# Kernel tuning notes

Measured on AMD Instinct MI355X. Metric: run time of the kernel, lower is better.

## Reference

```python
import jax, jax.numpy as jnp
import numpy as np
import math

B, L, IN_K, IN_V = 4, 2048, 256, 256
HID, HEADS, OUT = 1024, 8, 256
D = HID // HEADS  # head_dim = 128


def setup_inputs() -> dict:
    key = jax.random.key(0)
    ks = jax.random.split(key, 9)
    s = 0.02
    return {
        "KEY": jax.random.normal(ks[0], (B, L, IN_K), jnp.float32),
        "VALUE": jax.random.normal(ks[1], (B, L, IN_V), jnp.float32),
        "QUERY": jax.random.normal(ks[2], (B, L, IN_K), jnp.float32),
        "W_w": jax.random.normal(ks[3], (HID, IN_K), jnp.float32) * s,
        "W_b": jax.random.normal(ks[4], (HID,), jnp.float32) * s,
        "Wv_w": jax.random.normal(ks[5], (HID, IN_V), jnp.float32) * s,
        "Wv_b": jax.random.normal(ks[6], (HID,), jnp.float32) * s,
        "Wo_w": jax.random.normal(ks[7], (OUT, HID), jnp.float32) * s,
        "Wo_b": jax.random.normal(ks[8], (OUT,), jnp.float32) * s,
    }


def _split_heads(x, b, l):
    # reshape hidden -> (head_dim, num_heads) [head LAST, as in source], then
    # permute(0,3,1,2) -> [B, heads, L, head_dim]
    return x.reshape(b, l, D, HEADS).transpose(0, 3, 1, 2)


def reference(KEY, VALUE, QUERY, W_w, W_b, Wv_w, Wv_b, Wo_w, Wo_b):
    b, lk, _ = KEY.shape
    lq = QUERY.shape[1]
    # shared projection W for KEY and QUERY
    Wk = _split_heads(KEY @ W_w.T + W_b, b, lk)      # [B,h,Lk,d]
    Wq = _split_heads(QUERY @ W_w.T + W_b, b, lq)    # [B,h,Lq,d]
    Wv = _split_heads(VALUE @ Wv_w.T + Wv_b, b, lk)  # [B,h,Lk,d]
    # score[b,h,i,k] = sum_j Wk[b,h,i,j] * Wq[b,h,k,j]
    score = jnp.einsum('bhij,bhkj->bhik', Wk, Wq) / math.sqrt(D)
    # NON-STANDARD: softmax over the HEAD dimension (dim=1)
    attn = jax.nn.softmax(score, axis=1)             # [B,h,Lk,Lq]
    out = jnp.einsum('bhik,bhij->bhjk', attn, Wv)    # [B,h,d,Lq]
    out = out.transpose(0, 2, 1, 3)                  # [B,d,h,Lq]
    out = out.reshape(b, D * HEADS, lq)              # [B,hidden,Lq]
    out = jnp.swapaxes(out, 2, 1)                    # [B,Lq,hidden]
    # dropout is identity in eval mode
    return out @ Wo_w.T + Wo_b                       # [B,Lq,output_size]
```

## Files before the change

kernel.cpp:

```cpp
#include <hip/hip_runtime.h>
#include <hip/hip_bf16.h>
#include <stdint.h>

#define B_    4
#define L_    2048
#define INK   256
#define HID   1024
#define NH    8
#define DH    128
#define OUTF  256

typedef __bf16 v8bf __attribute__((ext_vector_type(8)));
typedef float  v4f  __attribute__((ext_vector_type(4)));

#define MFMA(a,b,c) __builtin_amdgcn_mfma_f32_16x16x32_bf16((a),(b),(c),0,0,0)

__device__ __forceinline__ void gl_lds16(const void* gsrc, void* ldsbase) {
  __builtin_amdgcn_global_load_lds(
      (const __attribute__((address_space(1))) unsigned int*)(uintptr_t)gsrc,
      (__attribute__((address_space(3))) unsigned int*)(uint32_t)(uintptr_t)ldsbase,
      16, 0, 0);
}
__device__ __forceinline__ void wait_vm0()  { asm volatile("s_waitcnt vmcnt(0)" ::: "memory"); }
__device__ __forceinline__ void wait_vm8()  { asm volatile("s_waitcnt vmcnt(8)" ::: "memory"); }
__device__ __forceinline__ void wait_lgkm0(){ asm volatile("s_waitcnt lgkmcnt(0)" ::: "memory"); }
__device__ __forceinline__ void barrier_lgkm() {
  asm volatile("s_waitcnt lgkmcnt(0)\n\ts_barrier" ::: "memory");
}

__device__ __forceinline__ unsigned short bfbits(float f) {
  __bf16 h = (__bf16)f;
  return __builtin_bit_cast(unsigned short, h);
}
__device__ __forceinline__ unsigned pack2(float a, float b) {
  return (unsigned)bfbits(a) | ((unsigned)bfbits(b) << 16);
}

struct ConvArgs {
  const float* src[5];
  __bf16* dst[5];
  int n[5];
};
__global__ __launch_bounds__(256)
void convert_kernel(ConvArgs a) {
  const int r = blockIdx.y;
  const int i = (blockIdx.x * 256 + threadIdx.x) * 4;
  if (i >= a.n[r]) return;
  const float4 v = *(const float4*)(a.src[r] + i);
  uint2 w;
  w.x = pack2(v.x, v.y);
  w.y = pack2(v.z, v.w);
  *reinterpret_cast<uint2*>(a.dst[r] + i) = w;
}

__global__ __launch_bounds__(256)
void wo_perm_kernel(const float* __restrict__ Wo, __bf16* __restrict__ Wop) {
  const int o = blockIdx.x;
  const int hidp = threadIdx.x * 4;
  const int h = hidp >> 7, dd = hidp & 127;
  const float* src = Wo + (size_t)o * HID;
  const float v0 = src[(dd + 0) * 8 + h];
  const float v1 = src[(dd + 1) * 8 + h];
  const float v2 = src[(dd + 2) * 8 + h];
  const float v3 = src[(dd + 3) * 8 + h];
  uint2 w;
  w.x = pack2(v0, v1);
  w.y = pack2(v2, v3);
  *reinterpret_cast<uint2*>(Wop + (size_t)o * HID + hidp) = w;
}

template<int MODE>
__global__ __launch_bounds__(256, 2)
void proj_kernel(const __bf16* __restrict__ X, const __bf16* __restrict__ W,
                 const float* __restrict__ bias, __bf16* __restrict__ out)
{
  __shared__ __bf16 sA[2][128 * 64];
  __shared__ __bf16 sB[2][128 * 64];
  const int tid  = threadIdx.x;
  const int lane = tid & 63;
  const int wid  = tid >> 6;
  const int l15  = lane & 15;
  const int q    = lane >> 4;
  const int mblk = blockIdx.x * 128;
  const int nblk = blockIdx.y * 128;

  v4f acc[4][4];
  const v4f vz = {0.f, 0.f, 0.f, 0.f};
#pragma unroll
  for (int i = 0; i < 4; i++)
#pragma unroll
    for (int j = 0; j < 4; j++) acc[i][j] = vz;

  const char* Ab = (const char*)X + (size_t)mblk * 512;
  const char* Bb = (const char*)W + (size_t)nblk * 512;

  auto stage = [&](int p, int c) {
    const int koff = c * 128;
#pragma unroll
    for (int j = 0; j < 4; j++) {
      const int slot = j * 256 + tid;
      const int row = slot >> 3, g = slot & 7;
      gl_lds16(Ab + (size_t)row * 512 + koff + ((g ^ (row & 7)) << 4),
               &sA[p][(j * 256 + wid * 64) * 8]);
    }
#pragma unroll
    for (int j = 0; j < 4; j++) {
      const int slot = j * 256 + tid;
      const int row = slot >> 3, g = slot & 7;
      gl_lds16(Bb + (size_t)row * 512 + koff + ((g ^ (row & 7)) << 4),
               &sB[p][(j * 256 + wid * 64) * 8]);
    }
  };

  stage(0, 0);
  __syncthreads();
#pragma unroll
  for (int c = 0; c < 4; c++) {
    const int p = c & 1;
    if (c + 1 < 4) stage(1 - p, c + 1);
#pragma unroll
    for (int s = 0; s < 2; s++) {
      v8bf a[4], b[4];
#pragma unroll
      for (int t = 0; t < 4; t++) {
        const int row = (wid & 1) * 64 + t * 16 + l15;
        a[t] = *(const v8bf*)&sA[p][(row << 6) + (((s * 4 + q) ^ (row & 7)) << 3)];
      }
#pragma unroll
      for (int t = 0; t < 4; t++) {
        const int row = (wid >> 1) * 64 + t * 16 + l15;
        b[t] = *(const v8bf*)&sB[p][(row << 6) + (((s * 4 + q) ^ (row & 7)) << 3)];
      }
#pragma unroll
      for (int tm = 0; tm < 4; tm++)
#pragma unroll
        for (int tn = 0; tn < 4; tn++)
          acc[tm][tn] = MFMA(a[tm], b[tn], acc[tm][tn]);
    }
    __syncthreads();
  }

#pragma unroll
  for (int tn = 0; tn < 4; tn++) {
    const int n = nblk + (wid >> 1) * 64 + tn * 16 + l15;
    const float bv = bias[n];
    const int h = n & 7;
    const int dd = n >> 3;
#pragma unroll
    for (int tm = 0; tm < 4; tm++)
#pragma unroll
      for (int r = 0; r < 4; r++) {
        const int m = mblk + (wid & 1) * 64 + tm * 16 + q * 4 + r;
        const int b = m >> 11;
        const int i = m & (L_ - 1);
        const float v = acc[tm][tn][r] + bv;
        size_t idx;
        if (MODE == 0) idx = ((size_t)(b * NH + h) * L_ + i) * DH + dd;
        else           idx = ((size_t)(b * NH + h) * DH + dd) * L_ + i;
        out[idx] = (__bf16)v;
      }
  }
}

__global__ __launch_bounds__(512, 2)
void fused_attn_kernel(const __bf16* __restrict__ Kp,
                       const __bf16* __restrict__ Qp,
                       const __bf16* __restrict__ Vpt,
                       __bf16* __restrict__ Hd)
{
  extern __shared__ char smem[];
  char* sK = smem;
  char* sV = smem + 65536;
  char* sP = smem + 131072;

  const int tid  = threadIdx.x;
  const int lane = tid & 63;
  const int h    = tid >> 6;
  const int l15  = lane & 15;
  const int q    = lane >> 4;
  const int k0   = blockIdx.x * 32;
  const int b    = blockIdx.y;

  const char* KpH = (const char*)Kp  + (size_t)(b * NH + h) * L_ * DH * 2;
  const char* QpH = (const char*)Qp  + (size_t)(b * NH + h) * L_ * DH * 2;
  const char* VpH = (const char*)Vpt + (size_t)(b * NH + h) * DH * L_ * 2;
  char* sKh = sK + h * 8192;
  char* sVh = sV + h * 8192;
  char* sPh = sP + h * 2048;

  auto stage_K = [&](int i0) {
#pragma unroll
    for (int j = 0; j < 8; j++) {
      const int slot = j * 64 + lane;
      const int row = slot >> 4, g = slot & 15;
      gl_lds16(KpH + (size_t)(i0 + row) * 256 + ((g ^ (row & 15)) << 4),
               sKh + j * 1024);
    }
  };
  auto stage_V = [&](int i0) {
#pragma unroll
    for (int j = 0; j < 8; j++) {
      const int slot = j * 64 + lane;
      const int row = slot >> 2, g = slot & 3;
      gl_lds16(VpH + (size_t)row * 4096 + (size_t)i0 * 2 + ((g ^ (row & 3)) << 4),
               sVh + j * 1024);
    }
  };

  stage_K(0);
  stage_V(0);

  v8bf qf[2][4];
#pragma unroll
  for (int n = 0; n < 2; n++)
#pragma unroll
    for (int c = 0; c < 4; c++)
      qf[n][c] = *(const v8bf*)(QpH + (size_t)(k0 + n * 16 + l15) * 256 + c * 64 + q * 16);

  v4f cacc[8][2];
  const v4f vz = {0.f, 0.f, 0.f, 0.f};
#pragma unroll
  for (int t = 0; t < 8; t++)
#pragma unroll
    for (int n = 0; n < 2; n++) cacc[t][n] = vz;

  const float c2 = 0.12751744f;
  const int ip = tid & 15;
  const int kk = tid >> 4;

  for (int it = 0; it < 64; ++it) {
    const int i0 = it * 32;
    wait_vm8();

    v8bf ka[2][4];
#pragma unroll
    for (int si = 0; si < 2; si++)
#pragma unroll
      for (int c = 0; c < 4; c++) {
        const int row = si * 16 + l15;
        ka[si][c] = *(const v8bf*)(sKh + row * 256 + (((c * 4 + q) ^ l15) << 4));
      }
    wait_lgkm0();
    if (it + 1 < 64) stage_K(i0 + 32);

    v4f s[2][2];
#pragma unroll
    for (int si = 0; si < 2; si++)
#pragma unroll
      for (int n = 0; n < 2; n++) s[si][n] = vz;
#pragma unroll
    for (int c = 0; c < 4; c++)
#pragma unroll
      for (int si = 0; si < 2; si++)
#pragma unroll
        for (int n = 0; n < 2; n++)
          s[si][n] = MFMA(ka[si][c], qf[n][c], s[si][n]);

#pragma unroll
    for (int si = 0; si < 2; si++)
#pragma unroll
      for (int n = 0; n < 2; n++) {
        const float p0 = exp2f(s[si][n][0] * c2);
        const float p1 = exp2f(s[si][n][1] * c2);
        const float p2 = exp2f(s[si][n][2] * c2);
        const float p3 = exp2f(s[si][n][3] * c2);
        uint2 w;
        w.x = pack2(p0, p1);
        w.y = pack2(p2, p3);
        *(uint2*)(sPh + (n * 16 + l15) * 64 + (si * 16 + q * 4) * 2) = w;
      }
    barrier_lgkm();

    {
      unsigned u[8];
      float lo[8], hi[8], s0 = 0.f, s1 = 0.f;
#pragma unroll
      for (int hh = 0; hh < 8; hh++)
        u[hh] = *(const unsigned*)(sP + hh * 2048 + kk * 64 + ip * 4);
#pragma unroll
      for (int hh = 0; hh < 8; hh++) {
        lo[hh] = __builtin_bit_cast(float, u[hh] << 16);
        hi[hh] = __builtin_bit_cast(float, u[hh] & 0xFFFF0000u);
        s0 += lo[hh];
        s1 += hi[hh];
      }
      const float r0 = __builtin_amdgcn_rcpf(s0);
      const float r1 = __builtin_amdgcn_rcpf(s1);
#pragma unroll
      for (int hh = 0; hh < 8; hh++)
        *(unsigned*)(sP + hh * 2048 + kk * 64 + ip * 4) = pack2(lo[hh] * r0, hi[hh] * r1);
    }
    barrier_lgkm();

    v8bf va[8], pb[2];
#pragma unroll
    for (int t = 0; t < 8; t++) {
      const int row = t * 16 + l15;
      va[t] = *(const v8bf*)(sVh + row * 64 + ((q ^ (row & 3)) << 4));
    }
#pragma unroll
    for (int n = 0; n < 2; n++)
      pb[n] = *(const v8bf*)(sPh + (n * 16 + l15) * 64 + q * 16);
    wait_lgkm0();
    if (it + 1 < 64) stage_V(i0 + 32);
    else wait_vm0();
#pragma unroll
    for (int t = 0; t < 8; t++)
#pragma unroll
      for (int n = 0; n < 2; n++)
        cacc[t][n] = MFMA(va[t], pb[n], cacc[t][n]);
  }

#pragma unroll
  for (int t = 0; t < 8; t++)
#pragma unroll
    for (int n = 0; n < 2; n++) {
      uint2 w;
      w.x = pack2(cacc[t][n][0], cacc[t][n][1]);
      w.y = pack2(cacc[t][n][2], cacc[t][n][3]);
      char* dst = (char*)Hd +
          (((size_t)(b * L_ + k0 + n * 16 + l15)) * HID + h * DH + t * 16 + q * 4) * 2;
      *(uint2*)dst = w;
    }
}

__global__ __launch_bounds__(256, 2)
void outproj_kernel(const __bf16* __restrict__ Hd, const __bf16* __restrict__ Wop,
                    const float* __restrict__ bo, float* __restrict__ out)
{
  __shared__ __bf16 sA[2][64 * 64];
  __shared__ __bf16 sB[2][64 * 64];
  const int tid  = threadIdx.x;
  const int lane = tid & 63;
  const int wid  = tid >> 6;
  const int l15  = lane & 15;
  const int q    = lane >> 4;
  const int mblk = blockIdx.x * 64;
  const int nblk = blockIdx.y * 64;

  const char* Ab = (const char*)Hd  + (size_t)mblk * 2048;
  const char* Bb = (const char*)Wop + (size_t)nblk * 2048;

  auto stage = [&](int p, int c) {
#pragma unroll
    for (int j = 0; j < 2; j++) {
      const int slot = j * 256 + tid;
      const int row = slot >> 3, g = slot & 7;
      gl_lds16(Ab + (size_t)row * 2048 + c * 128 + ((g ^ (row & 7)) << 4),
               &sA[p][(j * 256 + wid * 64) * 8]);
    }
#pragma unroll
    for (int j = 0; j < 2; j++) {
      const int slot = j * 256 + tid;
      const int row = slot >> 3, g = slot & 7;
      gl_lds16(Bb + (size_t)row * 2048 + c * 128 + ((g ^ (row & 7)) << 4),
               &sB[p][(j * 256 + wid * 64) * 8]);
    }
  };

  v4f acc[2][2];
  const v4f vz = {0.f, 0.f, 0.f, 0.f};
#pragma unroll
  for (int i = 0; i < 2; i++)
#pragma unroll
    for (int j = 0; j < 2; j++) acc[i][j] = vz;

  stage(0, 0);
  __syncthreads();
#pragma unroll 1
  for (int c = 0; c < 16; c++) {
    const int p = c & 1;
    if (c + 1 < 16) stage(1 - p, c + 1);
#pragma unroll
    for (int s = 0; s < 2; s++) {
      v8bf a[2], bb[2];
#pragma unroll
      for (int t = 0; t < 2; t++) {
        const int row = (wid & 1) * 32 + t * 16 + l15;
        a[t] = *(const v8bf*)&sA[p][(row << 6) + (((s * 4 + q) ^ (row & 7)) << 3)];
      }
#pragma unroll
      for (int t = 0; t < 2; t++) {
        const int row = (wid >> 1) * 32 + t * 16 + l15;
        bb[t] = *(const v8bf*)&sB[p][(row << 6) + (((s * 4 + q) ^ (row & 7)) << 3)];
      }
#pragma unroll
      for (int tm = 0; tm < 2; tm++)
#pragma unroll
        for (int tn = 0; tn < 2; tn++)
          acc[tm][tn] = MFMA(a[tm], bb[tn], acc[tm][tn]);
    }
    __syncthreads();
  }

#pragma unroll
  for (int tn = 0; tn < 2; tn++) {
    const int n = nblk + (wid >> 1) * 32 + tn * 16 + l15;
    const float bv = bo[n];
#pragma unroll
    for (int tm = 0; tm < 2; tm++)
#pragma unroll
      for (int r = 0; r < 4; r++) {
        const int m = mblk + (wid & 1) * 32 + tm * 16 + q * 4 + r;
        out[(size_t)m * OUTF + n] = acc[tm][tn][r] + bv;
      }
  }
}

extern "C" void kernel_launch(void* const* d_in, const int* in_sizes, int n_in,
                              void* d_out, int out_size, void* d_ws, size_t ws_size,
                              hipStream_t stream) {
  const float* KEY   = (const float*)d_in[0];
  const float* VALUE = (const float*)d_in[1];
  const float* QUERY = (const float*)d_in[2];
  const float* W_w   = (const float*)d_in[3];
  const float* W_b   = (const float*)d_in[4];
  const float* Wv_w  = (const float*)d_in[5];
  const float* Wv_b  = (const float*)d_in[6];
  const float* Wo_w  = (const float*)d_in[7];
  const float* Wo_b  = (const float*)d_in[8];
  float* out = (float*)d_out;

  const size_t MB = 1024 * 1024;
  char* ws = (char*)d_ws;
  __bf16* Kp  = (__bf16*)(ws);
  __bf16* Qp  = (__bf16*)(ws + 16 * MB);
  __bf16* Vpt = (__bf16*)(ws + 32 * MB);
  __bf16* Hd  = (__bf16*)(ws + 48 * MB);
  __bf16* Wop = (__bf16*)(ws + 64 * MB);
  __bf16* Xk  = (__bf16*)(ws + 48 * MB);
  __bf16* Xq  = (__bf16*)(ws + 48 * MB + 4 * MB);
  __bf16* Xv  = (__bf16*)(ws + 48 * MB + 8 * MB);
  __bf16* Wb  = (__bf16*)(ws + 48 * MB + 12 * MB);
  __bf16* Wvb = (__bf16*)(ws + 48 * MB + 12 * MB + 512 * 1024);

  ConvArgs ca;
  ca.src[0] = KEY;   ca.dst[0] = Xk;  ca.n[0] = B_ * L_ * INK;
  ca.src[1] = QUERY; ca.dst[1] = Xq;  ca.n[1] = B_ * L_ * INK;
  ca.src[2] = VALUE; ca.dst[2] = Xv;  ca.n[2] = B_ * L_ * INK;
  ca.src[3] = W_w;   ca.dst[3] = Wb;  ca.n[3] = HID * INK;
  ca.src[4] = Wv_w;  ca.dst[4] = Wvb; ca.n[4] = HID * INK;
  convert_kernel<<<dim3(2048, 5), 256, 0, stream>>>(ca);
  wo_perm_kernel<<<dim3(256), 256, 0, stream>>>(Wo_w, Wop);

  proj_kernel<0><<<dim3(64, 8), 256, 0, stream>>>(Xk, Wb,  W_b,  Kp);
  proj_kernel<0><<<dim3(64, 8), 256, 0, stream>>>(Xq, Wb,  W_b,  Qp);
  proj_kernel<1><<<dim3(64, 8), 256, 0, stream>>>(Xv, Wvb, Wv_b, Vpt);

  fused_attn_kernel<<<dim3(64, B_), 512, 147456, stream>>>(Kp, Qp, Vpt, Hd);

  outproj_kernel<<<dim3(128, 4), 256, 0, stream>>>(Hd, Wop, Wo_b, out);
}
```

Baseline: 348.5 us.

## Load K directly from global, double-buffer V in LDS, pad P rows

The attention kernel no longer stages K tiles through LDS; each wave reads its K fragments straight from global memory. The freed LDS becomes a second V buffer, so the next V tile is prefetched while the current one is consumed, and the per-iteration LDS wait before the V stage is removed. V is stored in a new unswizzled layout, and the P scratch rows are padded from 64 to 80 bytes to cut bank conflicts. LDS use grows to 148 KB, and the direct K loads are uncoalesced 16-byte global reads that may add latency to the score MFMAs.

```diff
diff --git a/kernel.cpp b/kernel.cpp
--- a/kernel.cpp
+++ b/kernel.cpp
@@ -23,7 +23,6 @@
 }
 __device__ __forceinline__ void wait_vm0()  { asm volatile("s_waitcnt vmcnt(0)" ::: "memory"); }
 __device__ __forceinline__ void wait_vm8()  { asm volatile("s_waitcnt vmcnt(8)" ::: "memory"); }
-__device__ __forceinline__ void wait_lgkm0(){ asm volatile("s_waitcnt lgkmcnt(0)" ::: "memory"); }
 __device__ __forceinline__ void barrier_lgkm() {
   asm volatile("s_waitcnt lgkmcnt(0)\n\ts_barrier" ::: "memory");
 }
@@ -169,8 +168,7 @@
                        __bf16* __restrict__ Hd)
 {
   extern __shared__ char smem[];
-  char* sK = smem;
-  char* sV = smem + 65536;
+  char* sV = smem;
   char* sP = smem + 131072;
 
   const int tid  = threadIdx.x;
@@ -184,31 +182,21 @@
   const char* KpH = (const char*)Kp  + (size_t)(b * NH + h) * L_ * DH * 2;
   const char* QpH = (const char*)Qp  + (size_t)(b * NH + h) * L_ * DH * 2;
   const char* VpH = (const char*)Vpt + (size_t)(b * NH + h) * DH * L_ * 2;
-  char* sKh = sK + h * 8192;
-  char* sVh = sV + h * 8192;
-  char* sPh = sP + h * 2048;
-
-  auto stage_K = [&](int i0) {
+  char* sPh = sP + h * 2560;
+
+  auto stage_V = [&](int p, int i0) {
+    char* sVp = sV + p * 65536 + h * 8192;
 #pragma unroll
     for (int j = 0; j < 8; j++) {
       const int slot = j * 64 + lane;
-      const int row = slot >> 4, g = slot & 15;
-      gl_lds16(KpH + (size_t)(i0 + row) * 256 + ((g ^ (row & 15)) << 4),
-               sKh + j * 1024);
+      const int dd = slot & 127;
+      const int ii = slot >> 7;
+      gl_lds16(VpH + (size_t)dd * 4096 + (size_t)i0 * 2 + ii * 16,
+               sVp + j * 1024);
     }
   };
-  auto stage_V = [&](int i0) {
-#pragma unroll
-    for (int j = 0; j < 8; j++) {
-      const int slot = j * 64 + lane;
-      const int row = slot >> 2, g = slot & 3;
-      gl_lds16(VpH + (size_t)row * 4096 + (size_t)i0 * 2 + ((g ^ (row & 3)) << 4),
-               sVh + j * 1024);
-    }
-  };
-
-  stage_K(0);
-  stage_V(0);
+
+  stage_V(0, 0);
 
   v8bf qf[2][4];
 #pragma unroll
@@ -230,18 +218,21 @@
 
   for (int it = 0; it < 64; ++it) {
     const int i0 = it * 32;
-    wait_vm8();
+    const int p = it & 1;
 
     v8bf ka[2][4];
 #pragma unroll
     for (int si = 0; si < 2; si++)
 #pragma unroll
-      for (int c = 0; c < 4; c++) {
-        const int row = si * 16 + l15;
-        ka[si][c] = *(const v8bf*)(sKh + row * 256 + (((c * 4 + q) ^ l15) << 4));
-      }
-    wait_lgkm0();
-    if (it + 1 < 64) stage_K(i0 + 32);
+      for (int c = 0; c < 4; c++)
+        ka[si][c] = *(const v8bf*)(KpH + (size_t)(i0 + si * 16 + l15) * 256 + (c * 4 + q) * 16);
+
+    if (it + 1 < 64) {
+      stage_V(1 - p, i0 + 32);
+      wait_vm8();
+    } else {
+      wait_vm0();
+    }
 
     v4f s[2][2];
 #pragma unroll
@@ -267,7 +258,7 @@
         uint2 w;
         w.x = pack2(p0, p1);
         w.y = pack2(p2, p3);
-        *(uint2*)(sPh + (n * 16 + l15) * 64 + (si * 16 + q * 4) * 2) = w;
+        *(uint2*)(sPh + (n * 16 + l15) * 80 + (si * 16 + q * 4) * 2) = w;
       }
     barrier_lgkm();
 
@@ -276,7 +267,7 @@
       float lo[8], hi[8], s0 = 0.f, s1 = 0.f;
 #pragma unroll
       for (int hh = 0; hh < 8; hh++)
-        u[hh] = *(const unsigned*)(sP + hh * 2048 + kk * 64 + ip * 4);
+        u[hh] = *(const unsigned*)(sP + hh * 2560 + kk * 80 + ip * 4);
 #pragma unroll
       for (int hh = 0; hh < 8; hh++) {
         lo[hh] = __builtin_bit_cast(float, u[hh] << 16);
@@ -288,27 +279,25 @@
       const float r1 = __builtin_amdgcn_rcpf(s1);
 #pragma unroll
       for (int hh = 0; hh < 8; hh++)
-        *(unsigned*)(sP + hh * 2048 + kk * 64 + ip * 4) = pack2(lo[hh] * r0, hi[hh] * r1);
+        *(unsigned*)(sP + hh * 2560 + kk * 80 + ip * 4) = pack2(lo[hh] * r0, hi[hh] * r1);
     }
     barrier_lgkm();
 
-    v8bf va[8], pb[2];
-#pragma unroll
-    for (int t = 0; t < 8; t++) {
-      const int row = t * 16 + l15;
-      va[t] = *(const v8bf*)(sVh + row * 64 + ((q ^ (row & 3)) << 4));
-    }
-#pragma unroll
-    for (int n = 0; n < 2; n++)
-      pb[n] = *(const v8bf*)(sPh + (n * 16 + l15) * 64 + q * 16);
-    wait_lgkm0();
-    if (it + 1 < 64) stage_V(i0 + 32);
-    else wait_vm0();
-#pragma unroll
-    for (int t = 0; t < 8; t++)
+    {
+      char* sVp = sV + p * 65536 + h * 8192;
+      v8bf va[8], pb[2];
+#pragma unroll
+      for (int t = 0; t < 8; t++)
+        va[t] = *(const v8bf*)(sVp + q * 2048 + (t * 16 + l15) * 16);
 #pragma unroll
       for (int n = 0; n < 2; n++)
-        cacc[t][n] = MFMA(va[t], pb[n], cacc[t][n]);
+        pb[n] = *(const v8bf*)(sPh + (n * 16 + l15) * 80 + q * 16);
+#pragma unroll
+      for (int t = 0; t < 8; t++)
+#pragma unroll
+        for (int n = 0; n < 2; n++)
+          cacc[t][n] = MFMA(va[t], pb[n], cacc[t][n]);
+    }
   }
 
 #pragma unroll
@@ -447,7 +436,7 @@
   proj_kernel<0><<<dim3(64, 8), 256, 0, stream>>>(Xq, Wb,  W_b,  Qp);
   proj_kernel<1><<<dim3(64, 8), 256, 0, stream>>>(Xv, Wvb, Wv_b, Vpt);
 
-  fused_attn_kernel<<<dim3(64, B_), 512, 147456, stream>>>(Kp, Qp, Vpt, Hd);
+  fused_attn_kernel<<<dim3(64, B_), 512, 151552, stream>>>(Kp, Qp, Vpt, Hd);
 
   outproj_kernel<<<dim3(128, 4), 256, 0, stream>>>(Hd, Wop, Wo_b, out);
 }
```

Result: slower. 554.1 us (+59.0%).
